# Kernel optimization log

Hardware: AMD Instinct MI355X
Metric: run time of the kernel (lower is better)

## Reference

```python
import jax, jax.numpy as jnp
import numpy as np

N_ROWS = 5000  # hard-coded loop bound in the source
N_FEAT = 20    # hard-coded x size in the source


def setup_inputs() -> dict:
    key = jax.random.key(0)
    kA, kb, kx = jax.random.split(key, 3)
    A = jax.random.normal(kA, (N_ROWS, N_FEAT), dtype=jnp.float32)
    b = jax.random.normal(kb, (N_ROWS,), dtype=jnp.float32)
    # nn.Parameter initialized as uniform(low=1, high=13, size=20)
    x = 1.0 + 12.0 * jax.random.uniform(kx, (N_FEAT,), dtype=jnp.float32)
    return {"A": A, "b": b, "x": x}


def reference(A, b, x):
    # Original: loss = sum_i ||A[i,:] @ x - b||^2, where the scalar A[i]@x
    # broadcasts against the full vector b each iteration.
    # Vectorized: s = A @ x (shape [N_ROWS]); residual r[i,j] = s[i] - b[j].
    s = A @ x                                   # [5000]
    r = s[:, None] - b[None, :]                  # [5000, 5000] broadcasted residual
    return jnp.sum(r * r)
```

## Files before the change

kernel.cpp:

```cpp
#include <hip/hip_runtime.h>
#include <hip/hip_bf16.h>


#define N_ROWS 5000
#define N_FEAT 20
#define BLKSZ  1024
#define NWAVES (BLKSZ / 64)

__device__ __forceinline__ double wave_reduce_sum(double v) {
    #pragma unroll
    for (int off = 32; off > 0; off >>= 1)
        v += __shfl_down(v, off, 64);
    return v;
}

__global__ __launch_bounds__(BLKSZ) void lsq_fused_kernel(
        const float* __restrict__ A, const float* __restrict__ b,
        const float* __restrict__ x, float* __restrict__ out) {
    __shared__ float xs[N_FEAT];
    if (threadIdx.x < N_FEAT) xs[threadIdx.x] = x[threadIdx.x];
    __syncthreads();

    float x0 = xs[0],  x1 = xs[1],  x2 = xs[2],  x3 = xs[3],  x4 = xs[4];
    float x5 = xs[5],  x6 = xs[6],  x7 = xs[7],  x8 = xs[8],  x9 = xs[9];
    float x10 = xs[10], x11 = xs[11], x12 = xs[12], x13 = xs[13], x14 = xs[14];
    float x15 = xs[15], x16 = xs[16], x17 = xs[17], x18 = xs[18], x19 = xs[19];

    double s1 = 0.0, s2 = 0.0, b1 = 0.0, b2 = 0.0;
    for (int i = threadIdx.x; i < N_ROWS; i += BLKSZ) {
        const float4* __restrict__ row = (const float4*)(A + (long)i * N_FEAT);
        float4 r0 = row[0], r1 = row[1], r2 = row[2], r3 = row[3], r4 = row[4];
        float bv = b[i];

        float s = r0.x * x0  + r0.y * x1  + r0.z * x2  + r0.w * x3
                + r1.x * x4  + r1.y * x5  + r1.z * x6  + r1.w * x7
                + r2.x * x8  + r2.y * x9  + r2.z * x10 + r2.w * x11
                + r3.x * x12 + r3.y * x13 + r3.z * x14 + r3.w * x15
                + r4.x * x16 + r4.y * x17 + r4.z * x18 + r4.w * x19;

        s1 += (double)s;
        s2 += (double)s * (double)s;
        b1 += (double)bv;
        b2 += (double)bv * (double)bv;
    }

    s1 = wave_reduce_sum(s1);
    s2 = wave_reduce_sum(s2);
    b1 = wave_reduce_sum(b1);
    b2 = wave_reduce_sum(b2);

    __shared__ double red[NWAVES][4];
    int lane = threadIdx.x & 63;
    int wave = threadIdx.x >> 6;
    if (lane == 0) {
        red[wave][0] = s1; red[wave][1] = s2;
        red[wave][2] = b1; red[wave][3] = b2;
    }
    __syncthreads();
    if (threadIdx.x == 0) {
        double t0 = 0, t1 = 0, t2 = 0, t3 = 0;
        #pragma unroll
        for (int w = 0; w < NWAVES; ++w) {
            t0 += red[w][0]; t1 += red[w][1];
            t2 += red[w][2]; t3 += red[w][3];
        }
        double n = (double)N_ROWS;
        out[0] = (float)(n * t1 - 2.0 * t0 * t2 + n * t3);
    }
}

extern "C" void kernel_launch(void* const* d_in, const int* in_sizes, int n_in,
                              void* d_out, int out_size, void* d_ws, size_t ws_size,
                              hipStream_t stream) {
    const float* A = (const float*)d_in[0];
    const float* b = (const float*)d_in[1];
    const float* x = (const float*)d_in[2];
    float* out = (float*)d_out;
    (void)d_ws; (void)ws_size;

    lsq_fused_kernel<<<1, BLKSZ, 0, stream>>>(A, b, x, out);
}
```

Before: 62.81 us.

## Split row reduction across 20 blocks with cooperative grid sync

```diff
diff --git a/kernel.cpp b/kernel.cpp
--- a/kernel.cpp
+++ b/kernel.cpp
@@ -1,10 +1,14 @@
 #include <hip/hip_runtime.h>
 #include <hip/hip_bf16.h>
+#include <hip/hip_cooperative_groups.h>
+
+namespace cg = cooperative_groups;
 
 
 #define N_ROWS 5000
 #define N_FEAT 20
-#define BLKSZ  1024
+#define NBLK   20
+#define BLKSZ  256
 #define NWAVES (BLKSZ / 64)
 
 __device__ __forceinline__ double wave_reduce_sum(double v) {
@@ -14,34 +18,29 @@
     return v;
 }
 
-__global__ __launch_bounds__(BLKSZ) void lsq_fused_kernel(
+__global__ __launch_bounds__(BLKSZ) void lsq_coop_kernel(
         const float* __restrict__ A, const float* __restrict__ b,
-        const float* __restrict__ x, float* __restrict__ out) {
+        const float* __restrict__ x, double* __restrict__ ws,
+        float* __restrict__ out) {
     __shared__ float xs[N_FEAT];
     if (threadIdx.x < N_FEAT) xs[threadIdx.x] = x[threadIdx.x];
     __syncthreads();
 
-    float x0 = xs[0],  x1 = xs[1],  x2 = xs[2],  x3 = xs[3],  x4 = xs[4];
-    float x5 = xs[5],  x6 = xs[6],  x7 = xs[7],  x8 = xs[8],  x9 = xs[9];
-    float x10 = xs[10], x11 = xs[11], x12 = xs[12], x13 = xs[13], x14 = xs[14];
-    float x15 = xs[15], x16 = xs[16], x17 = xs[17], x18 = xs[18], x19 = xs[19];
-
     double s1 = 0.0, s2 = 0.0, b1 = 0.0, b2 = 0.0;
-    for (int i = threadIdx.x; i < N_ROWS; i += BLKSZ) {
+    int i = blockIdx.x * BLKSZ + threadIdx.x;
+    if (i < N_ROWS) {
         const float4* __restrict__ row = (const float4*)(A + (long)i * N_FEAT);
         float4 r0 = row[0], r1 = row[1], r2 = row[2], r3 = row[3], r4 = row[4];
         float bv = b[i];
-
-        float s = r0.x * x0  + r0.y * x1  + r0.z * x2  + r0.w * x3
-                + r1.x * x4  + r1.y * x5  + r1.z * x6  + r1.w * x7
-                + r2.x * x8  + r2.y * x9  + r2.z * x10 + r2.w * x11
-                + r3.x * x12 + r3.y * x13 + r3.z * x14 + r3.w * x15
-                + r4.x * x16 + r4.y * x17 + r4.z * x18 + r4.w * x19;
-
-        s1 += (double)s;
-        s2 += (double)s * (double)s;
-        b1 += (double)bv;
-        b2 += (double)bv * (double)bv;
+        float s = r0.x * xs[0]  + r0.y * xs[1]  + r0.z * xs[2]  + r0.w * xs[3]
+                + r1.x * xs[4]  + r1.y * xs[5]  + r1.z * xs[6]  + r1.w * xs[7]
+                + r2.x * xs[8]  + r2.y * xs[9]  + r2.z * xs[10] + r2.w * xs[11]
+                + r3.x * xs[12] + r3.y * xs[13] + r3.z * xs[14] + r3.w * xs[15]
+                + r4.x * xs[16] + r4.y * xs[17] + r4.z * xs[18] + r4.w * xs[19];
+        s1 = (double)s;
+        s2 = (double)s * (double)s;
+        b1 = (double)bv;
+        b2 = (double)bv * (double)bv;
     }
 
     s1 = wave_reduce_sum(s1);
@@ -64,8 +63,29 @@
             t0 += red[w][0]; t1 += red[w][1];
             t2 += red[w][2]; t3 += red[w][3];
         }
-        double n = (double)N_ROWS;
-        out[0] = (float)(n * t1 - 2.0 * t0 * t2 + n * t3);
+        double* p = ws + 4 * blockIdx.x;
+        p[0] = t0; p[1] = t1; p[2] = t2; p[3] = t3;
+        __threadfence();
+    }
+
+    cg::this_grid().sync();
+
+    if (blockIdx.x == 0) {
+        double v1 = 0, v2 = 0, v3 = 0, v4 = 0;
+        if (threadIdx.x < NBLK) {
+            volatile const double* p = ws + 4 * threadIdx.x;
+            v1 = p[0]; v2 = p[1]; v3 = p[2]; v4 = p[3];
+        }
+        if (threadIdx.x < 64) {
+            v1 = wave_reduce_sum(v1);
+            v2 = wave_reduce_sum(v2);
+            v3 = wave_reduce_sum(v3);
+            v4 = wave_reduce_sum(v4);
+            if (threadIdx.x == 0) {
+                double n = (double)N_ROWS;
+                out[0] = (float)(n * v2 - 2.0 * v1 * v3 + n * v4);
+            }
+        }
     }
 }
 
@@ -75,8 +95,10 @@
     const float* A = (const float*)d_in[0];
     const float* b = (const float*)d_in[1];
     const float* x = (const float*)d_in[2];
+    double* ws = (double*)d_ws;
     float* out = (float*)d_out;
-    (void)d_ws; (void)ws_size;
 
-    lsq_fused_kernel<<<1, BLKSZ, 0, stream>>>(A, b, x, out);
+    void* args[] = {(void*)&A, (void*)&b, (void*)&x, (void*)&ws, (void*)&out};
+    hipLaunchCooperativeKernel((void*)lsq_coop_kernel, dim3(NBLK), dim3(BLKSZ),
+                               args, 0, stream);
 }
```

Result: slower. 82.65 us (+31.6%).
